# Kernel optimization log

Measured on AMD Instinct MI355X. Metric: run time of the kernel, lower is better.

The kernel has to match this reference:

```python
import jax, jax.numpy as jnp
import numpy as np

N_NODES = 50000
N_EDGES = 1600000
D = 128
N_LAYERS = 3
N_GRAPHS = 128


def setup_inputs() -> dict:
    key = jax.random.key(0)
    ks = jax.random.split(key, 6)
    x = jax.random.normal(ks[0], (N_NODES, D), dtype=jnp.float32)
    edge_index = jax.random.randint(ks[1], (2, N_EDGES), 0, N_NODES, dtype=jnp.int64)
    batch = jnp.sort(jax.random.randint(ks[2], (N_NODES,), 0, N_GRAPHS, dtype=jnp.int64))
    scale = 1.0 / np.sqrt(D)
    W_l = jax.random.normal(ks[3], (N_LAYERS, D, D), dtype=jnp.float32) * scale
    W_r = jax.random.normal(ks[4], (N_LAYERS, D, D), dtype=jnp.float32) * scale
    b = jnp.zeros((N_LAYERS, D), dtype=jnp.float32)
    return {"x": x, "edge_index": edge_index, "batch": batch,
            "W_l": W_l, "W_r": W_r, "b": b}


def reference(x, edge_index, batch, W_l, W_r, b):
    # PyG SAGEConv (aggr='mean', root_weight=True):
    #   out_i = W_l @ mean_{j in N(i)} x_j + W_r @ x_i + b
    src, dst = edge_index[0], edge_index[1]
    n = x.shape[0]
    deg = jax.ops.segment_sum(jnp.ones((src.shape[0],), x.dtype), dst,
                              num_segments=n)
    inv_deg = jnp.where(deg > 0, 1.0 / jnp.maximum(deg, 1.0), 0.0)[:, None]
    L = W_l.shape[0]
    for l in range(L):
        agg = jax.ops.segment_sum(x[src], dst, num_segments=n) * inv_deg  # [N, D]
        x = agg @ W_l[l] + x @ W_r[l] + b[l]
        if l < L - 1:
            x = jax.nn.relu(x)  # dropout is identity in eval mode
    # global_add_pool over graph ids
    out = jax.ops.segment_sum(x, batch, num_segments=N_GRAPHS)  # [G, D]
    return out
```

## Files before the change

### kernel.cpp

```cpp
#include <hip/hip_runtime.h>
#include <hip/hip_bf16.h>

#define N_NODES 50000
#define N_EDGES 1600000
#define DIM 128
#define N_LAYERS 3
#define N_GRAPHS 128

#define NBUCK 196
#define CAP   12288
#define T1    4096
#define G1    ((N_EDGES + T1 - 1) / T1)
#define ZROW  50000

#define CVT_BLKS 6250
#define PACK_BLKS 48

typedef __attribute__((ext_vector_type(8))) short bf16x8;
typedef __attribute__((ext_vector_type(4))) float f32x4;
typedef __attribute__((ext_vector_type(2))) float f32x2;
typedef __attribute__((ext_vector_type(4))) int i32x4;
typedef __attribute__((ext_vector_type(2))) unsigned int u32x2;

__device__ __forceinline__ unsigned short f2bfu(float f) {
    __hip_bfloat16 h = __float2bfloat16(f);
    return *reinterpret_cast<unsigned short*>(&h);
}
__device__ __forceinline__ void acc8(i32x4 v, float* a) {
    union { int i; float f; } t;
    t.i = v.x << 16;         a[0] += t.f;
    t.i = v.x & 0xffff0000;  a[1] += t.f;
    t.i = v.y << 16;         a[2] += t.f;
    t.i = v.y & 0xffff0000;  a[3] += t.f;
    t.i = v.z << 16;         a[4] += t.f;
    t.i = v.z & 0xffff0000;  a[5] += t.f;
    t.i = v.w << 16;         a[6] += t.f;
    t.i = v.w & 0xffff0000;  a[7] += t.f;
}
__device__ __forceinline__ void accf8(u32x2 w, float* a) {
    f32x2 p0 = __builtin_amdgcn_cvt_pk_f32_fp8((int)w.x, false);
    f32x2 p1 = __builtin_amdgcn_cvt_pk_f32_fp8((int)w.x, true);
    f32x2 p2 = __builtin_amdgcn_cvt_pk_f32_fp8((int)w.y, false);
    f32x2 p3 = __builtin_amdgcn_cvt_pk_f32_fp8((int)w.y, true);
    a[0] += p0.x; a[1] += p0.y; a[2] += p1.x; a[3] += p1.y;
    a[4] += p2.x; a[5] += p2.y; a[6] += p3.x; a[7] += p3.y;
}
__device__ __forceinline__ unsigned char f2fp8(float v) {
    return (unsigned char)(__builtin_amdgcn_cvt_pk_fp8_f32(v, v, 0, false) & 0xFF);
}

__global__ __launch_bounds__(256) void prep_kernel(const float4* __restrict__ x4,
                                                   const float* __restrict__ Wl,
                                                   const float* __restrict__ Wr,
                                                   ushort4* __restrict__ xb4,
                                                   unsigned int* __restrict__ xf8u,
                                                   unsigned short* __restrict__ wp,
                                                   int* __restrict__ cursor) {
    int bid = blockIdx.x;
    if (bid < CVT_BLKS) {
        int i = bid * 256 + threadIdx.x;
        float4 v = x4[i];
        ushort4 o;
        o.x = f2bfu(v.x); o.y = f2bfu(v.y); o.z = f2bfu(v.z); o.w = f2bfu(v.w);
        xb4[i] = o;
        int w = __builtin_amdgcn_cvt_pk_fp8_f32(v.x, v.y, 0, false);
        w = __builtin_amdgcn_cvt_pk_fp8_f32(v.z, v.w, w, true);
        xf8u[i] = (unsigned int)w;
        return;
    }
    if (bid < CVT_BLKS + PACK_BLKS) {
        int t = (bid - CVT_BLKS) * 256 + threadIdx.x;
        if (t >= 3 * 2 * 4 * 8 * 64) return;
        int lane = t & 63;
        int rest = t >> 6;
        int ct = rest & 7; rest >>= 3;
        int kt = rest & 3; rest >>= 2;
        int mat = rest & 1; rest >>= 1;
        int layer = rest;
        const float* W = (mat ? Wr : Wl) + (size_t)layer * DIM * DIM;
        int col = ct * 16 + (lane & 15);
        int k0 = kt * 32 + (lane >> 4) * 8;
        unsigned short* dst = wp + (size_t)t * 8;
#pragma unroll
        for (int j = 0; j < 8; j++) dst[j] = f2bfu(W[(k0 + j) * DIM + col]);
        return;
    }
    if (threadIdx.x < NBUCK) cursor[threadIdx.x] = threadIdx.x * CAP;
    if (threadIdx.x < 32) xf8u[(size_t)ZROW * 32 + threadIdx.x] = 0u;
}

__global__ __launch_bounds__(256) void pass1_partition(const int* __restrict__ ei,
                                                       int* __restrict__ cursor,
                                                       unsigned int* __restrict__ pairs) {
    __shared__ int h[256], sc[256], o[256], c[256], gb[256];
    __shared__ unsigned int stg[T1];
    int tid = threadIdx.x;
    int e0 = blockIdx.x * T1;
    int e1 = min(e0 + T1, N_EDGES);
    h[tid] = 0;
    __syncthreads();
    for (int e = e0 + tid; e < e1; e += 256) atomicAdd(&h[ei[N_EDGES + e] >> 8], 1);
    __syncthreads();
    int myc = h[tid];
    sc[tid] = myc;
    __syncthreads();
    for (int off = 1; off < 256; off <<= 1) {
        int t = (tid >= off) ? sc[tid - off] : 0;
        __syncthreads();
        sc[tid] += t;
        __syncthreads();
    }
    o[tid] = sc[tid] - myc;
    c[tid] = o[tid];
    __syncthreads();
    for (int e = e0 + tid; e < e1; e += 256) {
        unsigned int s = (unsigned int)ei[e];
        unsigned int d = (unsigned int)ei[N_EDGES + e];
        int p = atomicAdd(&c[d >> 8], 1);
        stg[p] = (d << 16) | s;
    }
    __syncthreads();
    if (tid < NBUCK && myc) gb[tid] = atomicAdd(&cursor[tid], myc);
    __syncthreads();
    int cnt = e1 - e0;
    for (int j = tid; j < cnt; j += 256) {
        unsigned int v = stg[j];
        int bk = v >> 24;
        pairs[gb[bk] + (j - o[bk])] = v;
    }
}

__global__ __launch_bounds__(256) void pass2_fill(const unsigned int* __restrict__ pairs,
                                                  const int* __restrict__ cursor,
                                                  unsigned int* __restrict__ rp,
                                                  float* __restrict__ inv_deg,
                                                  unsigned short* __restrict__ csr16) {
    __shared__ int lh[256], sc[256], lf[256];
    int tid = threadIdx.x;
    int b = blockIdx.x;
    int p0 = b * CAP, p1 = cursor[b];
    lh[tid] = 0;
    __syncthreads();
    for (int p = p0 + tid; p < p1; p += 256) atomicAdd(&lh[(pairs[p] >> 16) & 255], 1);
    __syncthreads();
    int deg = lh[tid];
    int pdeg = max(deg, lh[tid ^ 1]);
    int padL = (pdeg + 7) & ~7;
    sc[tid] = padL;
    __syncthreads();
    for (int off = 1; off < 256; off <<= 1) {
        int t = (tid >= off) ? sc[tid - off] : 0;
        __syncthreads();
        sc[tid] += t;
        __syncthreads();
    }
    int base = p0 + sc[tid] - padL;
    int node = (b << 8) + tid;
    if (node < N_NODES) {
        rp[node] = (unsigned int)base | ((unsigned int)deg << 24);
        inv_deg[node] = (deg > 0) ? 1.0f / (float)deg : 0.0f;
    }
    lf[tid] = base;
    __syncthreads();
    for (int k = deg; k < padL; k++) csr16[base + k] = (unsigned short)ZROW;
    for (int p = p0 + tid; p < p1; p += 256) {
        unsigned int v = pairs[p];
        int pos = atomicAdd(&lf[(v >> 16) & 255], 1);
        csr16[pos] = (unsigned short)(v & 0xFFFF);
    }
}

__global__ __launch_bounds__(256) void agg_kernel(const unsigned char* __restrict__ xf8,
                                                  const unsigned short* __restrict__ csr16,
                                                  const unsigned int* __restrict__ rp,
                                                  const float* __restrict__ inv_deg,
                                                  unsigned short* __restrict__ aggb) {
    int pairi = blockIdx.x * 4 + (threadIdx.x >> 6);
    int lane = threadIdx.x & 63;
    const int na   = lane >> 5;
    const int slot = (lane >> 4) & 1;
    const int sub  = lane & 15;
    int n0 = pairi * 2;
    unsigned int r0 = rp[n0], r1 = rp[n0 + 1];
    int s0 = r0 & 0xFFFFFF, s1 = r1 & 0xFFFFFF;
    int padL = s1 - s0;
    int myStart = na ? s1 : s0;
    float a[8] = {0.f, 0.f, 0.f, 0.f, 0.f, 0.f, 0.f, 0.f};
    int e = myStart + slot * 4;
    for (int it = 0; it < padL; it += 8) {
        ushort4 idx = *(const ushort4*)(csr16 + e);
        u32x2 v0 = *(const u32x2*)(xf8 + (size_t)idx.x * DIM + sub * 8);
        u32x2 v1 = *(const u32x2*)(xf8 + (size_t)idx.y * DIM + sub * 8);
        u32x2 v2 = *(const u32x2*)(xf8 + (size_t)idx.z * DIM + sub * 8);
        u32x2 v3 = *(const u32x2*)(xf8 + (size_t)idx.w * DIM + sub * 8);
        accf8(v0, a); accf8(v1, a); accf8(v2, a); accf8(v3, a);
        e += 8;
    }
#pragma unroll
    for (int k = 0; k < 8; k++) a[k] += __shfl_xor(a[k], 16);
    if (slot == 0) {
        int node = n0 + na;
        float w = inv_deg[node];
        i32x4 o;
        o.x = ((int)f2bfu(a[1] * w) << 16) | f2bfu(a[0] * w);
        o.y = ((int)f2bfu(a[3] * w) << 16) | f2bfu(a[2] * w);
        o.z = ((int)f2bfu(a[5] * w) << 16) | f2bfu(a[4] * w);
        o.w = ((int)f2bfu(a[7] * w) << 16) | f2bfu(a[6] * w);
        *(i32x4*)(aggb + (size_t)node * DIM + sub * 8) = o;
    }
}

template <int RELU, int WRITE_FP8>
__global__ __launch_bounds__(256) void gemm_mfma_kernel(
    const unsigned short* __restrict__ aggb,
    const unsigned short* __restrict__ xb,
    const unsigned short* __restrict__ wp,
    const float* __restrict__ bias,
    unsigned short* __restrict__ outb,
    unsigned char* __restrict__ outf8) {
    const int NT = N_NODES / 16;
    int wid = (blockIdx.x * blockDim.x + threadIdx.x) >> 6;
    int lane = threadIdx.x & 63;
    if (wid >= NT) return;
    const int R0 = wid * 16;
    const int l15 = lane & 15, l4 = lane >> 4;

    f32x4 acc[8];
#pragma unroll
    for (int c = 0; c < 8; c++) {
        float bv = bias[c * 16 + l15];
        acc[c] = (f32x4){bv, bv, bv, bv};
    }

#pragma unroll
    for (int mat = 0; mat < 2; mat++) {
        const unsigned short* src = mat ? xb : aggb;
        const unsigned short* wbase = wp + mat * (4 * 8 * 64 * 8);
#pragma unroll
        for (int kt = 0; kt < 4; kt++) {
            bf16x8 a0 = *(const bf16x8*)(src + (size_t)(R0 + l15) * DIM + kt * 32 + l4 * 8);
            const unsigned short* wk = wbase + kt * (8 * 64 * 8) + lane * 8;
#pragma unroll
            for (int c = 0; c < 8; c++) {
                bf16x8 bf = *(const bf16x8*)(wk + c * (64 * 8));
                acc[c] = __builtin_amdgcn_mfma_f32_16x16x32_bf16(a0, bf, acc[c], 0, 0, 0);
            }
        }
    }

    int r0 = R0 + l4 * 4;
#pragma unroll
    for (int c = 0; c < 8; c++) {
        int col = c * 16 + l15;
#pragma unroll
        for (int j = 0; j < 4; j++) {
            float v = acc[c][j];
            if (RELU) v = fmaxf(v, 0.f);
            outb[(size_t)(r0 + j) * DIM + col] = f2bfu(v);
            if (WRITE_FP8) outf8[(size_t)(r0 + j) * DIM + col] = f2fp8(v);
        }
    }
}

__global__ __launch_bounds__(1024) void pool_kernel(const unsigned short* __restrict__ xb,
                                                    const int* __restrict__ batch,
                                                    float* __restrict__ out) {
    __shared__ float red[16][DIM];
    int g = blockIdx.x;
    int tid = threadIdx.x;
    int wv = tid >> 6;
    int lane = tid & 63;
    int fo = lane & 15;
    int rs = lane >> 4;
    int lo = 0, hi = N_NODES;
    while (lo < hi) { int m = (lo + hi) >> 1; if (batch[m] < g) lo = m + 1; else hi = m; }
    int start = lo;
    lo = 0; hi = N_NODES;
    while (lo < hi) { int m = (lo + hi) >> 1; if (batch[m] < g + 1) lo = m + 1; else hi = m; }
    int end = lo;
    float a[8] = {0.f, 0.f, 0.f, 0.f, 0.f, 0.f, 0.f, 0.f};
    for (int r = start + wv * 4 + rs; r < end; r += 64) {
        i32x4 v = *(const i32x4*)(xb + (size_t)r * DIM + fo * 8);
        acc8(v, a);
    }
#pragma unroll
    for (int k = 0; k < 8; k++) {
        a[k] += __shfl_xor(a[k], 16);
        a[k] += __shfl_xor(a[k], 32);
    }
    if (rs == 0) {
#pragma unroll
        for (int k = 0; k < 8; k++) red[wv][fo * 8 + k] = a[k];
    }
    __syncthreads();
    if (tid < DIM) {
        float s = 0.f;
#pragma unroll
        for (int w = 0; w < 16; w++) s += red[w][tid];
        out[g * DIM + tid] = s;
    }
}

extern "C" void kernel_launch(void* const* d_in, const int* in_sizes, int n_in,
                              void* d_out, int out_size, void* d_ws, size_t ws_size,
                              hipStream_t stream) {
    const float* x   = (const float*)d_in[0];
    const int*   ei  = (const int*)d_in[1];
    const int*   bat = (const int*)d_in[2];
    const float* Wl  = (const float*)d_in[3];
    const float* Wr  = (const float*)d_in[4];
    const float* b   = (const float*)d_in[5];
    float* out = (float*)d_out;

    char* ws = (char*)d_ws;
    size_t off = 0;
    auto carve = [&](size_t bytes) {
        void* p = ws + off;
        off += (bytes + 255) & ~(size_t)255;
        return p;
    };
    int*            cursor  = (int*)carve(sizeof(int) * 256);
    unsigned int*   rp      = (unsigned int*)carve(sizeof(unsigned int) * N_NODES);
    unsigned short* csr16   = (unsigned short*)carve(sizeof(unsigned short) * NBUCK * CAP);
    float*          inv_deg = (float*)carve(sizeof(float) * N_NODES);
    unsigned char*  xf8     = (unsigned char*)carve(1ull * (N_NODES + 1) * DIM);
    unsigned short* xb      = (unsigned short*)carve(2ull * N_NODES * DIM);
    unsigned short* actA    = (unsigned short*)carve(2ull * N_NODES * DIM);
    unsigned short* actB    = (unsigned short*)carve(2ull * N_NODES * DIM);
    unsigned short* aggb    = (unsigned short*)carve(2ull * N_NODES * DIM);
    unsigned short* wpack   = (unsigned short*)carve(2ull * 3 * 2 * 4 * 8 * 64 * 8);
    unsigned int*   pairs  = (unsigned int*)actB;
    unsigned short* finalb = actA;
    (void)ws_size; (void)in_sizes; (void)n_in; (void)out_size;

    prep_kernel<<<CVT_BLKS + PACK_BLKS + 1, 256, 0, stream>>>(
        (const float4*)x, Wl, Wr, (ushort4*)xb, (unsigned int*)xf8, wpack, cursor);
    pass1_partition<<<G1, 256, 0, stream>>>(ei, cursor, pairs);
    pass2_fill<<<NBUCK, 256, 0, stream>>>(pairs, cursor, rp, inv_deg, csr16);

    const int aggGrid  = N_NODES / 2 / 4;
    const int gemmGrid = (N_NODES / 16 * 64 + 255) / 256;
    const size_t wlayer = 2ull * 4 * 8 * 64 * 8;

    agg_kernel<<<aggGrid, 256, 0, stream>>>(xf8, csr16, rp, inv_deg, aggb);
    gemm_mfma_kernel<1, 1><<<gemmGrid, 256, 0, stream>>>(aggb, xb, wpack + 0 * wlayer,
                                                         b + 0 * DIM, actA, xf8);
    agg_kernel<<<aggGrid, 256, 0, stream>>>(xf8, csr16, rp, inv_deg, aggb);
    gemm_mfma_kernel<1, 1><<<gemmGrid, 256, 0, stream>>>(aggb, actA, wpack + 1 * wlayer,
                                                         b + 1 * DIM, actB, xf8);
    agg_kernel<<<aggGrid, 256, 0, stream>>>(xf8, csr16, rp, inv_deg, aggb);
    gemm_mfma_kernel<0, 0><<<gemmGrid, 256, 0, stream>>>(aggb, actB, wpack + 2 * wlayer,
                                                         b + 2 * DIM, finalb, nullptr);

    pool_kernel<<<N_GRAPHS, 1024, 0, stream>>>(finalb, bat, out);
}
```

Measured before the change: 193.7 us.

## Fuse neighbor aggregation and MFMA GEMM into one per-layer kernel

Merges the gather-mean aggregation and the dual bf16 MFMA GEMM into one kernel per layer. Each 512-thread block aggregates 16 nodes into LDS, then each of its 8 waves computes one 16-column output tile. This removes the aggb round-trip through global memory and three kernel launches. Because a layer now reads the fp8 features while writing the next layer's, the fp8 buffer is double-buffered. The costs are a block-wide barrier between the gather and GEMM phases, and each block re-reading the full weight pack with less MFMA work per wave.

Result: slower. 202.9 us (+4.7%).

```diff
diff --git a/kernel.cpp b/kernel.cpp
--- a/kernel.cpp
+++ b/kernel.cpp
@@ -53,7 +53,8 @@
                                                    const float* __restrict__ Wl,
                                                    const float* __restrict__ Wr,
                                                    ushort4* __restrict__ xb4,
-                                                   unsigned int* __restrict__ xf8u,
+                                                   unsigned int* __restrict__ xf8uA,
+                                                   unsigned int* __restrict__ xf8uB,
                                                    unsigned short* __restrict__ wp,
                                                    int* __restrict__ cursor) {
     int bid = blockIdx.x;
@@ -65,7 +66,7 @@
         xb4[i] = o;
         int w = __builtin_amdgcn_cvt_pk_fp8_f32(v.x, v.y, 0, false);
         w = __builtin_amdgcn_cvt_pk_fp8_f32(v.z, v.w, w, true);
-        xf8u[i] = (unsigned int)w;
+        xf8uA[i] = (unsigned int)w;
         return;
     }
     if (bid < CVT_BLKS + PACK_BLKS) {
@@ -86,7 +87,10 @@
         return;
     }
     if (threadIdx.x < NBUCK) cursor[threadIdx.x] = threadIdx.x * CAP;
-    if (threadIdx.x < 32) xf8u[(size_t)ZROW * 32 + threadIdx.x] = 0u;
+    if (threadIdx.x < 32) {
+        xf8uA[(size_t)ZROW * 32 + threadIdx.x] = 0u;
+        xf8uB[(size_t)ZROW * 32 + threadIdx.x] = 0u;
+    }
 }
 
 __global__ __launch_bounds__(256) void pass1_partition(const int* __restrict__ ei,
@@ -170,95 +174,82 @@
     }
 }
 
-__global__ __launch_bounds__(256) void agg_kernel(const unsigned char* __restrict__ xf8,
-                                                  const unsigned short* __restrict__ csr16,
-                                                  const unsigned int* __restrict__ rp,
-                                                  const float* __restrict__ inv_deg,
-                                                  unsigned short* __restrict__ aggb) {
-    int pairi = blockIdx.x * 4 + (threadIdx.x >> 6);
-    int lane = threadIdx.x & 63;
-    const int na   = lane >> 5;
-    const int slot = (lane >> 4) & 1;
-    const int sub  = lane & 15;
-    int n0 = pairi * 2;
-    unsigned int r0 = rp[n0], r1 = rp[n0 + 1];
-    int s0 = r0 & 0xFFFFFF, s1 = r1 & 0xFFFFFF;
-    int padL = s1 - s0;
-    int myStart = na ? s1 : s0;
-    float a[8] = {0.f, 0.f, 0.f, 0.f, 0.f, 0.f, 0.f, 0.f};
-    int e = myStart + slot * 4;
-    for (int it = 0; it < padL; it += 8) {
-        ushort4 idx = *(const ushort4*)(csr16 + e);
-        u32x2 v0 = *(const u32x2*)(xf8 + (size_t)idx.x * DIM + sub * 8);
-        u32x2 v1 = *(const u32x2*)(xf8 + (size_t)idx.y * DIM + sub * 8);
-        u32x2 v2 = *(const u32x2*)(xf8 + (size_t)idx.z * DIM + sub * 8);
-        u32x2 v3 = *(const u32x2*)(xf8 + (size_t)idx.w * DIM + sub * 8);
-        accf8(v0, a); accf8(v1, a); accf8(v2, a); accf8(v3, a);
-        e += 8;
-    }
-#pragma unroll
-    for (int k = 0; k < 8; k++) a[k] += __shfl_xor(a[k], 16);
-    if (slot == 0) {
-        int node = n0 + na;
-        float w = inv_deg[node];
-        i32x4 o;
-        o.x = ((int)f2bfu(a[1] * w) << 16) | f2bfu(a[0] * w);
-        o.y = ((int)f2bfu(a[3] * w) << 16) | f2bfu(a[2] * w);
-        o.z = ((int)f2bfu(a[5] * w) << 16) | f2bfu(a[4] * w);
-        o.w = ((int)f2bfu(a[7] * w) << 16) | f2bfu(a[6] * w);
-        *(i32x4*)(aggb + (size_t)node * DIM + sub * 8) = o;
-    }
-}
-
 template <int RELU, int WRITE_FP8>
-__global__ __launch_bounds__(256) void gemm_mfma_kernel(
-    const unsigned short* __restrict__ aggb,
+__global__ __launch_bounds__(512) void fused_layer_kernel(
+    const unsigned char* __restrict__ xf8_in,
     const unsigned short* __restrict__ xb,
+    const unsigned short* __restrict__ csr16,
+    const unsigned int* __restrict__ rp,
+    const float* __restrict__ inv_deg,
     const unsigned short* __restrict__ wp,
     const float* __restrict__ bias,
     unsigned short* __restrict__ outb,
     unsigned char* __restrict__ outf8) {
-    const int NT = N_NODES / 16;
-    int wid = (blockIdx.x * blockDim.x + threadIdx.x) >> 6;
-    int lane = threadIdx.x & 63;
-    if (wid >= NT) return;
-    const int R0 = wid * 16;
+    __shared__ unsigned short sAgg[16][DIM + 8];
+    const int R0 = blockIdx.x * 16;
+    const int wv = threadIdx.x >> 6;
+    const int lane = threadIdx.x & 63;
+
+    {
+        const int na   = lane >> 5;
+        const int slot = (lane >> 4) & 1;
+        const int sub  = lane & 15;
+        int n0 = R0 + wv * 2;
+        unsigned int r0 = rp[n0], r1 = rp[n0 + 1];
+        int s0 = r0 & 0xFFFFFF, s1 = r1 & 0xFFFFFF;
+        int padL = s1 - s0;
+        int myStart = na ? s1 : s0;
+        float a[8] = {0.f, 0.f, 0.f, 0.f, 0.f, 0.f, 0.f, 0.f};
+        int e = myStart + slot * 4;
+        for (int it = 0; it < padL; it += 8) {
+            ushort4 idx = *(const ushort4*)(csr16 + e);
+            u32x2 v0 = *(const u32x2*)(xf8_in + (size_t)idx.x * DIM + sub * 8);
+            u32x2 v1 = *(const u32x2*)(xf8_in + (size_t)idx.y * DIM + sub * 8);
+            u32x2 v2 = *(const u32x2*)(xf8_in + (size_t)idx.z * DIM + sub * 8);
+            u32x2 v3 = *(const u32x2*)(xf8_in + (size_t)idx.w * DIM + sub * 8);
+            accf8(v0, a); accf8(v1, a); accf8(v2, a); accf8(v3, a);
+            e += 8;
+        }
+#pragma unroll
+        for (int k = 0; k < 8; k++) a[k] += __shfl_xor(a[k], 16);
+        if (slot == 0) {
+            float w = inv_deg[n0 + na];
+            i32x4 o;
+            o.x = ((int)f2bfu(a[1] * w) << 16) | f2bfu(a[0] * w);
+            o.y = ((int)f2bfu(a[3] * w) << 16) | f2bfu(a[2] * w);
+            o.z = ((int)f2bfu(a[5] * w) << 16) | f2bfu(a[4] * w);
+            o.w = ((int)f2bfu(a[7] * w) << 16) | f2bfu(a[6] * w);
+            *(i32x4*)(&sAgg[wv * 2 + na][sub * 8]) = o;
+        }
+    }
+    __syncthreads();
+
     const int l15 = lane & 15, l4 = lane >> 4;
-
-    f32x4 acc[8];
-#pragma unroll
-    for (int c = 0; c < 8; c++) {
-        float bv = bias[c * 16 + l15];
-        acc[c] = (f32x4){bv, bv, bv, bv};
-    }
-
-#pragma unroll
-    for (int mat = 0; mat < 2; mat++) {
-        const unsigned short* src = mat ? xb : aggb;
-        const unsigned short* wbase = wp + mat * (4 * 8 * 64 * 8);
-#pragma unroll
-        for (int kt = 0; kt < 4; kt++) {
-            bf16x8 a0 = *(const bf16x8*)(src + (size_t)(R0 + l15) * DIM + kt * 32 + l4 * 8);
-            const unsigned short* wk = wbase + kt * (8 * 64 * 8) + lane * 8;
-#pragma unroll
-            for (int c = 0; c < 8; c++) {
-                bf16x8 bf = *(const bf16x8*)(wk + c * (64 * 8));
-                acc[c] = __builtin_amdgcn_mfma_f32_16x16x32_bf16(a0, bf, acc[c], 0, 0, 0);
-            }
-        }
-    }
-
-    int r0 = R0 + l4 * 4;
-#pragma unroll
-    for (int c = 0; c < 8; c++) {
-        int col = c * 16 + l15;
-#pragma unroll
-        for (int j = 0; j < 4; j++) {
-            float v = acc[c][j];
-            if (RELU) v = fmaxf(v, 0.f);
-            outb[(size_t)(r0 + j) * DIM + col] = f2bfu(v);
-            if (WRITE_FP8) outf8[(size_t)(r0 + j) * DIM + col] = f2fp8(v);
-        }
+    float bv = bias[wv * 16 + l15];
+    f32x4 acc = (f32x4){bv, bv, bv, bv};
+
+#pragma unroll
+    for (int kt = 0; kt < 4; kt++) {
+        bf16x8 a0 = *(const bf16x8*)(&sAgg[l15][kt * 32 + l4 * 8]);
+        bf16x8 bf = *(const bf16x8*)(wp + kt * (8 * 64 * 8) + wv * (64 * 8) + lane * 8);
+        acc = __builtin_amdgcn_mfma_f32_16x16x32_bf16(a0, bf, acc, 0, 0, 0);
+    }
+    const unsigned short* wbase = wp + (4 * 8 * 64 * 8);
+#pragma unroll
+    for (int kt = 0; kt < 4; kt++) {
+        bf16x8 a0 = *(const bf16x8*)(xb + (size_t)(R0 + l15) * DIM + kt * 32 + l4 * 8);
+        bf16x8 bf = *(const bf16x8*)(wbase + kt * (8 * 64 * 8) + wv * (64 * 8) + lane * 8);
+        acc = __builtin_amdgcn_mfma_f32_16x16x32_bf16(a0, bf, acc, 0, 0, 0);
+    }
+
+    int r0w = R0 + l4 * 4;
+    int col = wv * 16 + l15;
+#pragma unroll
+    for (int j = 0; j < 4; j++) {
+        float v = acc[j];
+        if (RELU) v = fmaxf(v, 0.f);
+        outb[(size_t)(r0w + j) * DIM + col] = f2bfu(v);
+        if (WRITE_FP8) outf8[(size_t)(r0w + j) * DIM + col] = f2fp8(v);
     }
 }
 
@@ -323,34 +314,31 @@
     unsigned int*   rp      = (unsigned int*)carve(sizeof(unsigned int) * N_NODES);
     unsigned short* csr16   = (unsigned short*)carve(sizeof(unsigned short) * NBUCK * CAP);
     float*          inv_deg = (float*)carve(sizeof(float) * N_NODES);
-    unsigned char*  xf8     = (unsigned char*)carve(1ull * (N_NODES + 1) * DIM);
+    unsigned char*  xf8A    = (unsigned char*)carve(1ull * (N_NODES + 1) * DIM);
+    unsigned char*  xf8B    = (unsigned char*)carve(1ull * (N_NODES + 1) * DIM);
     unsigned short* xb      = (unsigned short*)carve(2ull * N_NODES * DIM);
     unsigned short* actA    = (unsigned short*)carve(2ull * N_NODES * DIM);
     unsigned short* actB    = (unsigned short*)carve(2ull * N_NODES * DIM);
-    unsigned short* aggb    = (unsigned short*)carve(2ull * N_NODES * DIM);
     unsigned short* wpack   = (unsigned short*)carve(2ull * 3 * 2 * 4 * 8 * 64 * 8);
     unsigned int*   pairs  = (unsigned int*)actB;
     unsigned short* finalb = actA;
     (void)ws_size; (void)in_sizes; (void)n_in; (void)out_size;
 
     prep_kernel<<<CVT_BLKS + PACK_BLKS + 1, 256, 0, stream>>>(
-        (const float4*)x, Wl, Wr, (ushort4*)xb, (unsigned int*)xf8, wpack, cursor);
+        (const float4*)x, Wl, Wr, (ushort4*)xb,
+        (unsigned int*)xf8A, (unsigned int*)xf8B, wpack, cursor);
     pass1_partition<<<G1, 256, 0, stream>>>(ei, cursor, pairs);
     pass2_fill<<<NBUCK, 256, 0, stream>>>(pairs, cursor, rp, inv_deg, csr16);
 
-    const int aggGrid  = N_NODES / 2 / 4;
-    const int gemmGrid = (N_NODES / 16 * 64 + 255) / 256;
+    const int fusedGrid = N_NODES / 16;
     const size_t wlayer = 2ull * 4 * 8 * 64 * 8;
 
-    agg_kernel<<<aggGrid, 256, 0, stream>>>(xf8, csr16, rp, inv_deg, aggb);
-    gemm_mfma_kernel<1, 1><<<gemmGrid, 256, 0, stream>>>(aggb, xb, wpack + 0 * wlayer,
-                                                         b + 0 * DIM, actA, xf8);
-    agg_kernel<<<aggGrid, 256, 0, stream>>>(xf8, csr16, rp, inv_deg, aggb);
-    gemm_mfma_kernel<1, 1><<<gemmGrid, 256, 0, stream>>>(aggb, actA, wpack + 1 * wlayer,
-                                                         b + 1 * DIM, actB, xf8);
-    agg_kernel<<<aggGrid, 256, 0, stream>>>(xf8, csr16, rp, inv_deg, aggb);
-    gemm_mfma_kernel<0, 0><<<gemmGrid, 256, 0, stream>>>(aggb, actB, wpack + 2 * wlayer,
-                                                         b + 2 * DIM, finalb, nullptr);
+    fused_layer_kernel<1, 1><<<fusedGrid, 512, 0, stream>>>(
+        xf8A, xb, csr16, rp, inv_deg, wpack + 0 * wlayer, b + 0 * DIM, actA, xf8B);
+    fused_layer_kernel<1, 1><<<fusedGrid, 512, 0, stream>>>(
+        xf8B, actA, csr16, rp, inv_deg, wpack + 1 * wlayer, b + 1 * DIM, actB, xf8A);
+    fused_layer_kernel<0, 0><<<fusedGrid, 512, 0, stream>>>(
+        xf8A, actB, csr16, rp, inv_deg, wpack + 2 * wlayer, b + 2 * DIM, finalb, nullptr);
 
     pool_kernel<<<N_GRAPHS, 1024, 0, stream>>>(finalb, bat, out);
 }
```
